# Kernel tuning notes

Measured on AMD Instinct MI355X. Metric: run time of the kernel, lower is better.

Reference implementation:

```python
import jax, jax.numpy as jnp
import numpy as np

EPS = 1e-5      # numerical floor for degrees / std / attenuation
LEAK = 0.01     # LeakyReLU slope of mixing FCLayer
AVG_D = 3.3     # log(avg_degree + 1) from init_kwargs
BIG = 1e30      # masking constant for max/min aggregators


def setup_inputs() -> dict:
    key = jax.random.key(0)
    ks = jax.random.split(key, 12)
    B, N, Din, De, H = 8, 256, 128, 64, 128
    s = 0.05
    inp = {
        "input": jax.random.normal(ks[0], (B, N, Din), jnp.float32),
        "adj": (jax.random.uniform(ks[1], (B, N, N)) < 0.1).astype(jnp.float32),
        "adj_features": jax.random.normal(ks[2], (B, N, N, De), jnp.float32),
        "hidden": jnp.zeros((B * N, H), jnp.float32),
        "pre_W": jax.random.normal(ks[3], (2 * Din + De, Din), jnp.float32) * s,
        "pre_b": jnp.zeros((Din,), jnp.float32),
        "post_W": jax.random.normal(ks[4], (13 * Din, H), jnp.float32) * s,
        "post_b": jnp.zeros((H,), jnp.float32),
        "mix_W": jax.random.normal(ks[5], (H, H), jnp.float32) * s,
        "mix_b": jnp.zeros((H,), jnp.float32),
        "gru_Wih": jax.random.normal(ks[6], (3 * H, H), jnp.float32) * s,
        "gru_Whh": jax.random.normal(ks[7], (3 * H, H), jnp.float32) * s,
    }
    return inp


def reference(input, adj, adj_features, hidden, pre_W, pre_b, post_W, post_b,
              mix_W, mix_b, gru_Wih, gru_Whh):
    B, N, Din = input.shape
    H = mix_W.shape[1]
    # --- pretrans MLP over all pairs: Linear([h_i, h_j, e_ij]) ---
    # split the weight into blocks so we never materialize h_cat (B,N,N,2Din+De)
    Wi, Wj, We = pre_W[:Din], pre_W[Din:2 * Din], pre_W[2 * Din:]
    hi = input @ Wi            # (B,N,Din)
    hj = input @ Wj            # (B,N,Din)
    h_mod = (hi[:, :, None, :] + hj[:, None, :, :]
             + jnp.einsum('bije,ek->bijk', adj_features, We) + pre_b)  # (B,N,N,Din)
    # --- multi-aggregator masked reduction over source axis j ---
    deg = jnp.sum(adj, axis=2)                       # (B,N)
    degc = jnp.maximum(deg, EPS)[..., None]          # (B,N,1)
    s1 = jnp.einsum('bij,bijk->bik', adj, h_mod)
    s2 = jnp.einsum('bij,bijk->bik', adj, h_mod * h_mod)
    mean = s1 / degc
    var = jnp.maximum(s2 / degc - mean * mean, 0.0)
    std = jnp.sqrt(var + EPS)
    mask = adj[..., None] > 0
    has_nb = (deg > 0)[..., None]
    mx = jnp.where(has_nb, jnp.max(jnp.where(mask, h_mod, -BIG), axis=2), 0.0)
    mn = jnp.where(has_nb, jnp.min(jnp.where(mask, h_mod, BIG), axis=2), 0.0)
    m = jnp.concatenate([mean, mx, mn, std], axis=2)  # (B,N,4*Din)
    # --- scalers: identity, amplification, attenuation ---
    slog = (jnp.log(deg + 1.0) / AVG_D)[..., None]    # (B,N,1)
    m = jnp.concatenate([m, m * slog, m / (slog + EPS)], axis=2)  # (B,N,12*Din)
    # --- posttrans Linear + mixing FCLayer (LeakyReLU) ---
    m_cat = jnp.concatenate([input, m], axis=2)       # (B,N,13*Din)
    y = m_cat @ post_W + post_b                       # (B,N,H)
    y = y @ mix_W + mix_b
    y = jnp.where(y > 0, y, LEAK * y)
    # --- GRUCell (bias=False), torch gate order r,z,n ---
    x = y.reshape(B * N, H)
    gi = x @ gru_Wih.T
    gh = hidden @ gru_Whh.T
    r = jax.nn.sigmoid(gi[:, :H] + gh[:, :H])
    z = jax.nn.sigmoid(gi[:, H:2 * H] + gh[:, H:2 * H])
    n = jnp.tanh(gi[:, 2 * H:] + r * gh[:, 2 * H:])
    h_new = (1.0 - z) * n + z * hidden
    return h_new.reshape(B, N, H)
```

## Files before the change

kernel.cpp:

```cpp
#include <hip/hip_runtime.h>
#include <cstdint>
#include <cstddef>

#define EPSF 1e-5f
#define LEAKF 0.01f
#define AVGD 3.3f

static constexpr int Nn = 256, DIN = 128, DE = 64, Hn = 128;
static constexpr int BN = 2048;
static constexpr int CTA = 640;
static constexpr int CTW = 1664;

typedef short bf16x8 __attribute__((ext_vector_type(8)));
typedef float f32x4  __attribute__((ext_vector_type(4)));
union BF8 { bf16x8 v; uint16_t u[8]; };

__device__ __forceinline__ float bf2f(uint16_t u) { return __uint_as_float(((uint32_t)u) << 16); }
__device__ __forceinline__ float bflo(uint32_t u)  { return __uint_as_float(u << 16); }
__device__ __forceinline__ uint16_t f2bf(float f) {
  uint32_t u = __float_as_uint(f);
  u += 0x7fffu + ((u >> 16) & 1u);
  return (uint16_t)(u >> 16);
}

__device__ __forceinline__ int detect_bf16(const uint32_t* w) {
  float lo = bflo(w[threadIdx.x & 63]);
  unsigned long long ok = __ballot(fabsf(lo) < 64.f);
  return ok == 0xFFFFFFFFFFFFFFFFull;
}
__device__ __forceinline__ float loadf(const void* p, size_t i, int isbf) {
  return isbf ? bf2f(((const uint16_t*)p)[i]) : ((const float*)p)[i];
}
__device__ __forceinline__ f32x4 mfma16(bf16x8 a, bf16x8 b, f32x4 c) {
  return __builtin_amdgcn_mfma_f32_16x16x32_bf16(a, b, c, 0, 0, 0);
}

__global__ __launch_bounds__(256) void k_prep(
    const void* __restrict__ input, const void* __restrict__ pre_W,
    const void* __restrict__ post_W, const void* __restrict__ mix_W,
    const void* __restrict__ Wih, const void* __restrict__ Whh,
    const void* __restrict__ hidden, const void* __restrict__ pre_b,
    uint16_t* __restrict__ preWTb, uint16_t* __restrict__ postTb,
    uint16_t* __restrict__ mixTb, uint16_t* __restrict__ Wihb,
    uint16_t* __restrict__ Whhb, uint16_t* __restrict__ hidb,
    uint16_t* __restrict__ Ab, float* __restrict__ hi, float* __restrict__ hj) {
  int isbf = detect_bf16((const uint32_t*)input);
  int b = blockIdx.x, tid = threadIdx.x;
  if (b < 264) {
    __shared__ float tile[32][33];
    const void* src; int R, C, t; uint16_t* bdst;
    if (b < 16)       { src = mix_W;  R = 128;  C = 128; t = b;       bdst = mixTb; }
    else if (b < 224) { src = post_W; R = 1664; C = 128; t = b - 16;  bdst = postTb; }
    else              { src = pre_W;  R = 320;  C = 128; t = b - 224; bdst = preWTb; }
    int bx = t & 3, by = t >> 2;
    int tx = tid & 31, ty = tid >> 5;
    int c0 = bx * 32, r0 = by * 32;
    #pragma unroll
    for (int dy = 0; dy < 32; dy += 8) {
      size_t idx = (size_t)(r0 + ty + dy) * C + (c0 + tx);
      tile[ty + dy][tx] = loadf(src, idx, isbf);
    }
    __syncthreads();
    #pragma unroll
    for (int dy = 0; dy < 32; dy += 8)
      bdst[(size_t)(c0 + ty + dy) * R + (r0 + tx)] = f2bf(tile[tx][ty + dy]);
  } else if (b < 440) {
    const void* src; uint16_t* dst; int base;
    if (b < 288)      { src = Wih;    dst = Wihb; base = (b - 264) * 2048; }
    else if (b < 312) { src = Whh;    dst = Whhb; base = (b - 288) * 2048; }
    else              { src = hidden; dst = hidb; base = (b - 312) * 2048; }
    int i = base + tid * 8;
    uint16_t v[8];
    if (isbf) *(uint4*)v = *(const uint4*)((const uint16_t*)src + i);
    else { const float* s = (const float*)src + i;
           #pragma unroll
           for (int e = 0; e < 8; e++) v[e] = f2bf(s[e]); }
    *(uint4*)(dst + i) = *(uint4*)v;
  } else if (b < 568) {
    int idx = (b - 440) * 2048 + tid * 8;
    int node = idx >> 7, col = idx & 127;
    uint16_t v[8];
    if (isbf) *(uint4*)v = *(const uint4*)((const uint16_t*)input + idx);
    else { const float* s = (const float*)input + idx;
           #pragma unroll
           for (int e = 0; e < 8; e++) v[e] = f2bf(s[e]); }
    *(uint4*)(Ab + (size_t)node * CTA + col) = *(uint4*)v;
  } else {
    int lane = tid & 63, w = tid >> 6;
    int wg = (b - 568) * 4 + w;
    int rt = wg >> 4, nt = wg & 15;
    int ishj = nt >> 3, ct = nt & 7;
    int m16 = lane & 15, quad = lane >> 4;
    int col = ct * 16 + m16;
    int row = rt * 16 + m16;
    int kbase = ishj ? 128 : 0;
    f32x4 acc = {0.f, 0.f, 0.f, 0.f};
    #pragma unroll
    for (int kt = 0; kt < 4; kt++) {
      bf16x8 av;
      if (isbf) av = *(const bf16x8*)((const uint16_t*)input + (size_t)row * 128 + kt * 32 + quad * 8);
      else { const float* s = (const float*)input + (size_t)row * 128 + kt * 32 + quad * 8;
             BF8 t;
             #pragma unroll
             for (int e = 0; e < 8; e++) t.u[e] = f2bf(s[e]);
             av = t.v; }
      BF8 bb;
      #pragma unroll
      for (int j = 0; j < 8; j++) {
        size_t wi = (size_t)(kbase + kt * 32 + quad * 8 + j) * 128 + col;
        bb.u[j] = isbf ? ((const uint16_t*)pre_W)[wi] : f2bf(((const float*)pre_W)[wi]);
      }
      acc = mfma16(av, bb.v, acc);
    }
    float bias = ishj ? 0.f : loadf(pre_b, col, isbf);
    float* dst = ishj ? hj : hi;
    #pragma unroll
    for (int r = 0; r < 4; r++)
      dst[(size_t)(rt * 16 + quad * 4 + r) * 128 + col] = acc[r] + bias;
  }
}

__global__ __launch_bounds__(256) void k2_mfma(
    const void* __restrict__ input, const void* __restrict__ adj_raw,
    const void* __restrict__ af_raw,
    const float* __restrict__ hi, const float* __restrict__ hj,
    const uint16_t* __restrict__ preWTb, uint16_t* __restrict__ Ab,
    float* __restrict__ degw) {
  __shared__ int nbr[Nn];
  __shared__ int wcnt[4];
  int isbf = detect_bf16((const uint32_t*)input);
  int bi = blockIdx.x, tid = threadIdx.x;
  int lane = tid & 63, w = tid >> 6;

  float a = loadf(adj_raw, (size_t)bi * Nn + tid, isbf);
  unsigned long long bm = __ballot(a > 0.f);
  int pre = __popcll(bm & ((1ull << lane) - 1ull));
  if (lane == 0) wcnt[w] = __popcll(bm);
  __syncthreads();
  int base = 0, cnt = 0;
  #pragma unroll
  for (int i = 0; i < 4; i++) { if (i < w) base += wcnt[i]; cnt += wcnt[i]; }
  if (a > 0.f) nbr[base + pre] = tid;
  __syncthreads();

  int m16 = lane & 15, quad = lane >> 4;
  int col0 = w * 32 + m16, col1 = col0 + 16;

  bf16x8 b00 = *(const bf16x8*)&preWTb[(size_t)col0 * 320 + 256 + quad * 8];
  bf16x8 b01 = *(const bf16x8*)&preWTb[(size_t)col0 * 320 + 288 + quad * 8];
  bf16x8 b10 = *(const bf16x8*)&preWTb[(size_t)col1 * 320 + 256 + quad * 8];
  bf16x8 b11 = *(const bf16x8*)&preWTb[(size_t)col1 * 320 + 288 + quad * 8];

  float base0 = hi[(size_t)bi * 128 + col0];
  float base1 = hi[(size_t)bi * 128 + col1];
  const float* hjb = &hj[(size_t)(bi & ~(Nn - 1)) * 128];

  float s1a = 0.f, s2a = 0.f, mxa = -1e30f, mna = 1e30f;
  float s1b = 0.f, s2b = 0.f, mxb = -1e30f, mnb = 1e30f;

  for (int ce = 0; ce < cnt; ce += 16) {
    int ei = ce + m16; if (ei >= cnt) ei = cnt - 1;
    int j = nbr[ei];
    bf16x8 a0, a1;
    if (isbf) {
      const uint16_t* ar = (const uint16_t*)af_raw + ((size_t)bi * Nn + j) * DE;
      a0 = *(const bf16x8*)(ar + quad * 8);
      a1 = *(const bf16x8*)(ar + 32 + quad * 8);
    } else {
      const float* ar = (const float*)af_raw + ((size_t)bi * Nn + j) * DE;
      BF8 t0, t1;
      #pragma unroll
      for (int e = 0; e < 8; e++) {
        t0.u[e] = f2bf(ar[quad * 8 + e]);
        t1.u[e] = f2bf(ar[32 + quad * 8 + e]);
      }
      a0 = t0.v; a1 = t1.v;
    }
    float hjv0[4], hjv1[4]; int vld[4];
    #pragma unroll
    for (int r = 0; r < 4; r++) {
      int e = ce + quad * 4 + r;
      vld[r] = (e < cnt);
      int jj = nbr[vld[r] ? e : (cnt - 1)];
      hjv0[r] = hjb[(size_t)jj * 128 + col0];
      hjv1[r] = hjb[(size_t)jj * 128 + col1];
    }
    f32x4 C0 = {0.f,0.f,0.f,0.f}, C1 = C0;
    C0 = mfma16(a0, b00, C0); C0 = mfma16(a1, b01, C0);
    C1 = mfma16(a0, b10, C1); C1 = mfma16(a1, b11, C1);
    #pragma unroll
    for (int r = 0; r < 4; r++) {
      float h0 = base0 + hjv0[r] + C0[r];
      float h1 = base1 + hjv1[r] + C1[r];
      if (vld[r]) {
        s1a += h0; s2a += h0 * h0; mxa = fmaxf(mxa, h0); mna = fminf(mna, h0);
        s1b += h1; s2b += h1 * h1; mxb = fmaxf(mxb, h1); mnb = fminf(mnb, h1);
      }
    }
  }
  #pragma unroll
  for (int off = 16; off <= 32; off <<= 1) {
    s1a += __shfl_xor(s1a, off); s2a += __shfl_xor(s2a, off);
    mxa = fmaxf(mxa, __shfl_xor(mxa, off)); mna = fminf(mna, __shfl_xor(mna, off));
    s1b += __shfl_xor(s1b, off); s2b += __shfl_xor(s2b, off);
    mxb = fmaxf(mxb, __shfl_xor(mxb, off)); mnb = fminf(mnb, __shfl_xor(mnb, off));
  }
  if (tid == 0) degw[bi] = (float)cnt;
  if (quad == 0) {
    float degc = fmaxf((float)cnt, EPSF);
    uint16_t* mo = Ab + (size_t)bi * CTA + 128;
    #pragma unroll
    for (int t = 0; t < 2; t++) {
      float s1 = t ? s1b : s1a, s2 = t ? s2b : s2a;
      float mx = t ? mxb : mxa, mn = t ? mnb : mna;
      int col = t ? col1 : col0;
      float mean = s1 / degc;
      float var  = fmaxf(s2 / degc - mean * mean, 0.f);
      float stdv = sqrtf(var + EPSF);
      if (cnt == 0) { mx = 0.f; mn = 0.f; }
      mo[0*128+col] = f2bf(mean); mo[1*128+col] = f2bf(mx);
      mo[2*128+col] = f2bf(mn);   mo[3*128+col] = f2bf(stdv);
    }
  }
}

__global__ __launch_bounds__(256) void k3f(
    const uint16_t* __restrict__ Ab, const uint16_t* __restrict__ postTb,
    const void* __restrict__ post_b, const uint16_t* __restrict__ mixTb,
    const void* __restrict__ mix_b, const uint16_t* __restrict__ Wihb,
    const uint16_t* __restrict__ Whhb, const uint16_t* __restrict__ hidb,
    const float* __restrict__ degw, const void* __restrict__ input_flag,
    void* __restrict__ out) {
  constexpr int SX = 136;
  __shared__ __align__(16) uint16_t y_s[8 * SX];
  __shared__ __align__(16) uint16_t x_s[8 * SX];
  __shared__ __align__(16) uint16_t hid_s[8 * SX];
  int isbf = detect_bf16((const uint32_t*)input_flag);
  int tid = threadIdx.x;
  int n0 = blockIdx.x * 8;
  if (tid < 128) {
    int row = tid >> 4, c = (tid & 15) * 8;
    *(uint4*)&hid_s[row * SX + c] = *(const uint4*)&hidb[(size_t)(n0 + row) * 128 + c];
  }
  int lane = tid & 63, w = tid >> 6;
  int m16 = lane & 15, quad = lane >> 4;
  const uint16_t* ap = Ab + (size_t)(n0 + (m16 & 7)) * CTA + quad * 8;
  int col0 = (w * 2) * 16 + m16, col1 = (w * 2 + 1) * 16 + m16;
  const uint16_t* bp0 = postTb + (size_t)col0 * CTW + quad * 8;
  const uint16_t* bp1 = postTb + (size_t)col1 * CTW + quad * 8;

  f32x4 aX0 = {0.f,0.f,0.f,0.f}, aX1 = aX0;
  f32x4 a10 = aX0, a11 = aX0, a20 = aX0, a21 = aX0, a30 = aX0, a31 = aX0;
  #pragma unroll
  for (int kt = 0; kt < 4; kt++) {
    bf16x8 a = *(const bf16x8*)(ap + kt * 32);
    aX0 = mfma16(a, *(const bf16x8*)(bp0 + kt * 32), aX0);
    aX1 = mfma16(a, *(const bf16x8*)(bp1 + kt * 32), aX1);
  }
  #pragma unroll 4
  for (int kk = 0; kk < 16; kk++) {
    bf16x8 a = *(const bf16x8*)(ap + 128 + kk * 32);
    a10 = mfma16(a, *(const bf16x8*)(bp0 + 128  + kk * 32), a10);
    a20 = mfma16(a, *(const bf16x8*)(bp0 + 640  + kk * 32), a20);
    a30 = mfma16(a, *(const bf16x8*)(bp0 + 1152 + kk * 32), a30);
    a11 = mfma16(a, *(const bf16x8*)(bp1 + 128  + kk * 32), a11);
    a21 = mfma16(a, *(const bf16x8*)(bp1 + 640  + kk * 32), a21);
    a31 = mfma16(a, *(const bf16x8*)(bp1 + 1152 + kk * 32), a31);
  }
  float pb0 = loadf(post_b, col0, isbf), pb1 = loadf(post_b, col1, isbf);
  #pragma unroll
  for (int r = 0; r < 4; r++) {
    int row = quad * 4 + r;
    if (row < 8) {
      float deg = degw[n0 + row];
      float slog = logf(deg + 1.f) / AVGD;
      float inv  = 1.f / (slog + EPSF);
      y_s[row * SX + col0] = f2bf(aX0[r] + a10[r] + slog * a20[r] + inv * a30[r] + pb0);
      y_s[row * SX + col1] = f2bf(aX1[r] + a11[r] + slog * a21[r] + inv * a31[r] + pb1);
    }
  }
  __syncthreads();

  const uint16_t* ya = &y_s[(m16 & 7) * SX + quad * 8];
  const uint16_t* mb0 = mixTb + (size_t)col0 * 128 + quad * 8;
  const uint16_t* mb1 = mixTb + (size_t)col1 * 128 + quad * 8;
  f32x4 mm0 = {0.f,0.f,0.f,0.f}, mm1 = mm0;
  #pragma unroll
  for (int kt = 0; kt < 4; kt++) {
    bf16x8 a = *(const bf16x8*)(ya + kt * 32);
    mm0 = mfma16(a, *(const bf16x8*)(mb0 + kt * 32), mm0);
    mm1 = mfma16(a, *(const bf16x8*)(mb1 + kt * 32), mm1);
  }
  float mbias0 = loadf(mix_b, col0, isbf), mbias1 = loadf(mix_b, col1, isbf);
  #pragma unroll
  for (int r = 0; r < 4; r++) {
    int row = quad * 4 + r;
    if (row < 8) {
      float v0 = mm0[r] + mbias0; v0 = v0 > 0.f ? v0 : LEAKF * v0;
      float v1 = mm1[r] + mbias1; v1 = v1 > 0.f ? v1 : LEAKF * v1;
      x_s[row * SX + col0] = f2bf(v0);
      x_s[row * SX + col1] = f2bf(v1);
    }
  }
  __syncthreads();

  f32x4 gi[3][2], gh[3][2];
  #pragma unroll
  for (int q = 0; q < 3; q++)
    #pragma unroll
    for (int t = 0; t < 2; t++) { gi[q][t] = {0.f,0.f,0.f,0.f}; gh[q][t] = {0.f,0.f,0.f,0.f}; }
  const uint16_t* xa = &x_s[(m16 & 7) * SX + quad * 8];
  const uint16_t* ha = &hid_s[(m16 & 7) * SX + quad * 8];
  #pragma unroll
  for (int kt = 0; kt < 4; kt++) {
    bf16x8 ax = *(const bf16x8*)(xa + kt * 32);
    bf16x8 ah = *(const bf16x8*)(ha + kt * 32);
    #pragma unroll
    for (int q = 0; q < 3; q++) {
      gi[q][0] = mfma16(ax, *(const bf16x8*)&Wihb[(size_t)(q * 128 + col0) * 128 + kt * 32 + quad * 8], gi[q][0]);
      gi[q][1] = mfma16(ax, *(const bf16x8*)&Wihb[(size_t)(q * 128 + col1) * 128 + kt * 32 + quad * 8], gi[q][1]);
      gh[q][0] = mfma16(ah, *(const bf16x8*)&Whhb[(size_t)(q * 128 + col0) * 128 + kt * 32 + quad * 8], gh[q][0]);
      gh[q][1] = mfma16(ah, *(const bf16x8*)&Whhb[(size_t)(q * 128 + col1) * 128 + kt * 32 + quad * 8], gh[q][1]);
    }
  }
  #pragma unroll
  for (int t = 0; t < 2; t++) {
    int col = t ? col1 : col0;
    #pragma unroll
    for (int r = 0; r < 4; r++) {
      int row = quad * 4 + r;
      if (row < 8) {
        float rg = 1.f / (1.f + expf(-(gi[0][t][r] + gh[0][t][r])));
        float zg = 1.f / (1.f + expf(-(gi[1][t][r] + gh[1][t][r])));
        float ng = tanhf(gi[2][t][r] + rg * gh[2][t][r]);
        float hv = bf2f(hid_s[row * SX + col]);
        float res = (1.f - zg) * ng + zg * hv;
        size_t oi = (size_t)(n0 + row) * 128 + col;
        if (isbf) ((uint16_t*)out)[oi] = f2bf(res);
        else      ((float*)out)[oi]    = res;
      }
    }
  }
}

extern "C" void kernel_launch(void* const* d_in, const int* in_sizes, int n_in,
                              void* d_out, int out_size, void* d_ws, size_t ws_size,
                              hipStream_t stream) {
  const void* input  = d_in[0];
  const void* adj    = d_in[1];
  const void* af     = d_in[2];
  const void* hidden = d_in[3];
  const void* pre_W  = d_in[4];
  const void* pre_b  = d_in[5];
  const void* post_W = d_in[6];
  const void* post_b = d_in[7];
  const void* mix_W  = d_in[8];
  const void* mix_b  = d_in[9];
  const void* Wih    = d_in[10];
  const void* Whh    = d_in[11];

  float* ws = (float*)d_ws;
  float* hi   = ws;
  float* hj   = hi + 262144;
  float* degw = hj + 262144;
  uint16_t* Ab     = (uint16_t*)(degw + 2048);
  uint16_t* postTb = Ab + (size_t)BN * CTA;
  uint16_t* mixTb  = postTb + 212992;
  uint16_t* preWTb = mixTb + 16384;
  uint16_t* Wihb   = preWTb + 40960;
  uint16_t* Whhb   = Wihb + 49152;
  uint16_t* hidb   = Whhb + 49152;

  k_prep<<<1080, 256, 0, stream>>>(input, pre_W, post_W, mix_W, Wih, Whh, hidden, pre_b,
                                   preWTb, postTb, mixTb, Wihb, Whhb, hidb, Ab, hi, hj);
  k2_mfma<<<BN, 256, 0, stream>>>(input, adj, af, hi, hj, preWTb, Ab, degw);
  k3f<<<256, 256, 0, stream>>>(Ab, postTb, post_b, mixTb, mix_b,
                               Wihb, Whhb, hidb, degw, input, d_out);
}
```

Measured before the change: 239.5 us.

## Stage edge features via double-buffered LDS and halve rows per k3f block

In k2_mfma, the gathered edge-feature rows are now loaded cooperatively by 128 threads into a double-buffered shared-memory tile. The next chunk is prefetched while the current chunk is computed, replacing the per-wave redundant global loads in which all four waves fetched the same rows. This adds a block barrier per 16-edge chunk. Separately, k3f processes 4 rows per block instead of 8 and launches 512 blocks for more parallelism, at the cost of reading each weight tile twice as often and leaving more of each MFMA tile unused.

```diff
diff --git a/kernel.cpp b/kernel.cpp
--- a/kernel.cpp
+++ b/kernel.cpp
@@ -128,6 +128,7 @@
     float* __restrict__ degw) {
   __shared__ int nbr[Nn];
   __shared__ int wcnt[4];
+  __shared__ __align__(16) uint16_t buf[2][16 * 72];
   int isbf = detect_bf16((const uint32_t*)input);
   int bi = blockIdx.x, tid = threadIdx.x;
   int lane = tid & 63, w = tid >> 6;
@@ -158,44 +159,53 @@
   float s1a = 0.f, s2a = 0.f, mxa = -1e30f, mna = 1e30f;
   float s1b = 0.f, s2b = 0.f, mxb = -1e30f, mnb = 1e30f;
 
-  for (int ce = 0; ce < cnt; ce += 16) {
-    int ei = ce + m16; if (ei >= cnt) ei = cnt - 1;
-    int j = nbr[ei];
-    bf16x8 a0, a1;
-    if (isbf) {
-      const uint16_t* ar = (const uint16_t*)af_raw + ((size_t)bi * Nn + j) * DE;
-      a0 = *(const bf16x8*)(ar + quad * 8);
-      a1 = *(const bf16x8*)(ar + 32 + quad * 8);
-    } else {
-      const float* ar = (const float*)af_raw + ((size_t)bi * Nn + j) * DE;
-      BF8 t0, t1;
+  auto stage = [&](int ce, int sel) {
+    if (tid < 128) {
+      int e = tid >> 3, seg = tid & 7;
+      int ei = ce + e; if (ei >= cnt) ei = cnt - 1;
+      int j = nbr[ei];
+      uint16_t v[8];
+      if (isbf)
+        *(uint4*)v = *(const uint4*)((const uint16_t*)af_raw + ((size_t)bi * Nn + j) * DE + seg * 8);
+      else {
+        const float* s = (const float*)af_raw + ((size_t)bi * Nn + j) * DE + seg * 8;
+        #pragma unroll
+        for (int x = 0; x < 8; x++) v[x] = f2bf(s[x]);
+      }
+      *(uint4*)&buf[sel][e * 72 + seg * 8] = *(uint4*)v;
+    }
+  };
+
+  if (cnt > 0) {
+    stage(0, 0);
+    __syncthreads();
+    for (int ce = 0; ce < cnt; ce += 16) {
+      int cur = (ce >> 4) & 1;
+      if (ce + 16 < cnt) stage(ce + 16, cur ^ 1);
+      float hjv0[4], hjv1[4]; int vld[4];
       #pragma unroll
-      for (int e = 0; e < 8; e++) {
-        t0.u[e] = f2bf(ar[quad * 8 + e]);
-        t1.u[e] = f2bf(ar[32 + quad * 8 + e]);
-      }
-      a0 = t0.v; a1 = t1.v;
-    }
-    float hjv0[4], hjv1[4]; int vld[4];
-    #pragma unroll
-    for (int r = 0; r < 4; r++) {
-      int e = ce + quad * 4 + r;
-      vld[r] = (e < cnt);
-      int jj = nbr[vld[r] ? e : (cnt - 1)];
-      hjv0[r] = hjb[(size_t)jj * 128 + col0];
-      hjv1[r] = hjb[(size_t)jj * 128 + col1];
-    }
-    f32x4 C0 = {0.f,0.f,0.f,0.f}, C1 = C0;
-    C0 = mfma16(a0, b00, C0); C0 = mfma16(a1, b01, C0);
-    C1 = mfma16(a0, b10, C1); C1 = mfma16(a1, b11, C1);
-    #pragma unroll
-    for (int r = 0; r < 4; r++) {
-      float h0 = base0 + hjv0[r] + C0[r];
-      float h1 = base1 + hjv1[r] + C1[r];
-      if (vld[r]) {
-        s1a += h0; s2a += h0 * h0; mxa = fmaxf(mxa, h0); mna = fminf(mna, h0);
-        s1b += h1; s2b += h1 * h1; mxb = fmaxf(mxb, h1); mnb = fminf(mnb, h1);
-      }
+      for (int r = 0; r < 4; r++) {
+        int e = ce + quad * 4 + r;
+        vld[r] = (e < cnt);
+        int jj = nbr[vld[r] ? e : (cnt - 1)];
+        hjv0[r] = hjb[(size_t)jj * 128 + col0];
+        hjv1[r] = hjb[(size_t)jj * 128 + col1];
+      }
+      bf16x8 a0 = *(const bf16x8*)&buf[cur][m16 * 72 + quad * 8];
+      bf16x8 a1 = *(const bf16x8*)&buf[cur][m16 * 72 + 32 + quad * 8];
+      f32x4 C0 = {0.f,0.f,0.f,0.f}, C1 = C0;
+      C0 = mfma16(a0, b00, C0); C0 = mfma16(a1, b01, C0);
+      C1 = mfma16(a0, b10, C1); C1 = mfma16(a1, b11, C1);
+      #pragma unroll
+      for (int r = 0; r < 4; r++) {
+        float h0 = base0 + hjv0[r] + C0[r];
+        float h1 = base1 + hjv1[r] + C1[r];
+        if (vld[r]) {
+          s1a += h0; s2a += h0 * h0; mxa = fmaxf(mxa, h0); mna = fminf(mna, h0);
+          s1b += h1; s2b += h1 * h1; mxb = fmaxf(mxb, h1); mnb = fminf(mnb, h1);
+        }
+      }
+      __syncthreads();
     }
   }
   #pragma unroll
@@ -232,19 +242,19 @@
     const float* __restrict__ degw, const void* __restrict__ input_flag,
     void* __restrict__ out) {
   constexpr int SX = 136;
-  __shared__ __align__(16) uint16_t y_s[8 * SX];
-  __shared__ __align__(16) uint16_t x_s[8 * SX];
-  __shared__ __align__(16) uint16_t hid_s[8 * SX];
+  __shared__ __align__(16) uint16_t y_s[4 * SX];
+  __shared__ __align__(16) uint16_t x_s[4 * SX];
+  __shared__ __align__(16) uint16_t hid_s[4 * SX];
   int isbf = detect_bf16((const uint32_t*)input_flag);
   int tid = threadIdx.x;
-  int n0 = blockIdx.x * 8;
-  if (tid < 128) {
+  int n0 = blockIdx.x * 4;
+  if (tid < 64) {
     int row = tid >> 4, c = (tid & 15) * 8;
     *(uint4*)&hid_s[row * SX + c] = *(const uint4*)&hidb[(size_t)(n0 + row) * 128 + c];
   }
   int lane = tid & 63, w = tid >> 6;
   int m16 = lane & 15, quad = lane >> 4;
-  const uint16_t* ap = Ab + (size_t)(n0 + (m16 & 7)) * CTA + quad * 8;
+  const uint16_t* ap = Ab + (size_t)(n0 + (m16 & 3)) * CTA + quad * 8;
   int col0 = (w * 2) * 16 + m16, col1 = (w * 2 + 1) * 16 + m16;
   const uint16_t* bp0 = postTb + (size_t)col0 * CTW + quad * 8;
   const uint16_t* bp1 = postTb + (size_t)col1 * CTW + quad * 8;
@@ -271,7 +281,7 @@
   #pragma unroll
   for (int r = 0; r < 4; r++) {
     int row = quad * 4 + r;
-    if (row < 8) {
+    if (row < 4) {
       float deg = degw[n0 + row];
       float slog = logf(deg + 1.f) / AVGD;
       float inv  = 1.f / (slog + EPSF);
@@ -281,7 +291,7 @@
   }
   __syncthreads();
 
-  const uint16_t* ya = &y_s[(m16 & 7) * SX + quad * 8];
+  const uint16_t* ya = &y_s[(m16 & 3) * SX + quad * 8];
   const uint16_t* mb0 = mixTb + (size_t)col0 * 128 + quad * 8;
   const uint16_t* mb1 = mixTb + (size_t)col1 * 128 + quad * 8;
   f32x4 mm0 = {0.f,0.f,0.f,0.f}, mm1 = mm0;
@@ -295,7 +305,7 @@
   #pragma unroll
   for (int r = 0; r < 4; r++) {
     int row = quad * 4 + r;
-    if (row < 8) {
+    if (row < 4) {
       float v0 = mm0[r] + mbias0; v0 = v0 > 0.f ? v0 : LEAKF * v0;
       float v1 = mm1[r] + mbias1; v1 = v1 > 0.f ? v1 : LEAKF * v1;
       x_s[row * SX + col0] = f2bf(v0);
@@ -309,8 +319,8 @@
   for (int q = 0; q < 3; q++)
     #pragma unroll
     for (int t = 0; t < 2; t++) { gi[q][t] = {0.f,0.f,0.f,0.f}; gh[q][t] = {0.f,0.f,0.f,0.f}; }
-  const uint16_t* xa = &x_s[(m16 & 7) * SX + quad * 8];
-  const uint16_t* ha = &hid_s[(m16 & 7) * SX + quad * 8];
+  const uint16_t* xa = &x_s[(m16 & 3) * SX + quad * 8];
+  const uint16_t* ha = &hid_s[(m16 & 3) * SX + quad * 8];
   #pragma unroll
   for (int kt = 0; kt < 4; kt++) {
     bf16x8 ax = *(const bf16x8*)(xa + kt * 32);
@@ -329,7 +339,7 @@
     #pragma unroll
     for (int r = 0; r < 4; r++) {
       int row = quad * 4 + r;
-      if (row < 8) {
+      if (row < 4) {
         float rg = 1.f / (1.f + expf(-(gi[0][t][r] + gh[0][t][r])));
         float zg = 1.f / (1.f + expf(-(gi[1][t][r] + gh[1][t][r])));
         float ng = tanhf(gi[2][t][r] + rg * gh[2][t][r]);
@@ -374,6 +384,6 @@
   k_prep<<<1080, 256, 0, stream>>>(input, pre_W, post_W, mix_W, Wih, Whh, hidden, pre_b,
                                    preWTb, postTb, mixTb, Wihb, Whhb, hidb, Ab, hi, hj);
   k2_mfma<<<BN, 256, 0, stream>>>(input, adj, af, hi, hj, preWTb, Ab, degw);
-  k3f<<<256, 256, 0, stream>>>(Ab, postTb, post_b, mixTb, mix_b,
+  k3f<<<512, 256, 0, stream>>>(Ab, postTb, post_b, mixTb, mix_b,
                                Wihb, Whhb, hidb, degw, input, d_out);
 }
```

New measurement: 252.4 us. +5.4%, slower.
